# Kernel optimization log

Hardware: AMD Instinct MI355X
Metric: run time of the kernel (lower is better)

## Reference

```python
import jax, jax.numpy as jnp
import numpy as np

# dims
B, N = 8, 64            # graphs, nodes per graph (equal-size ragged batch)
IN_DIM, EDGE_DIM = 16, 8
D, H = 128, 4
DH = D // H             # 32
L = 3                   # num_layers
FF = 4 * D              # 512
OUT = 1
SCALE = float(np.sqrt(DH))


def setup_inputs() -> dict:
    key = jax.random.key(0)
    ks = jax.random.split(key, 24)
    w = lambda k, s: jax.random.normal(k, s, jnp.float32) * 0.02
    return {
        'x': jax.random.normal(ks[0], (B, N, IN_DIM), jnp.float32),
        'edge_attr': jax.random.normal(ks[1], (B, N, N, EDGE_DIM), jnp.float32),
        'edge_mask': jax.random.bernoulli(ks[2], 0.2, (B, N, N)),
        # feature encoder (linear node + linear edge encoders, learned no-edge token)
        'node_W': w(ks[3], (IN_DIM, D)), 'node_b': jnp.zeros((D,), jnp.float32),
        'edge_W': w(ks[4], (EDGE_DIM, D)), 'edge_b': jnp.zeros((D,), jnp.float32),
        'no_edge': w(ks[5], (D,)),
        # per-layer edge-transformer params (stacked over L for lax.scan)
        'Wq': w(ks[6], (L, D, D)), 'Wk': w(ks[7], (L, D, D)),
        'Wv1': w(ks[8], (L, D, D)), 'Wv2': w(ks[9], (L, D, D)),
        'Wo': w(ks[10], (L, D, D)), 'bo': jnp.zeros((L, D), jnp.float32),
        'ln1_g': jnp.ones((L, D), jnp.float32), 'ln1_b': jnp.zeros((L, D), jnp.float32),
        'W1': w(ks[11], (L, D, FF)), 'b1': jnp.zeros((L, FF), jnp.float32),
        'W2': w(ks[12], (L, FF, D)), 'b2': jnp.zeros((L, D), jnp.float32),
        'ln2_g': jnp.ones((L, D), jnp.float32), 'ln2_b': jnp.zeros((L, D), jnp.float32),
        'Wout': w(ks[13], (D, OUT)), 'bout': jnp.zeros((OUT,), jnp.float32),
    }


def _ln(t, g, b):
    m = t.mean(-1, keepdims=True)
    v = t.var(-1, keepdims=True)
    return (t - m) * jax.lax.rsqrt(v + 1e-5) * g + b


def _forward(x, edge_attr, edge_mask, node_W, node_b, edge_W, edge_b, no_edge,
             Wq, Wk, Wv1, Wv2, Wo, bo, ln1_g, ln1_b, W1, b1, W2, b2,
             ln2_g, ln2_b, Wout, bout):
    # feature encoding: pair-token grid [B,N,N,D]
    node_emb = x @ node_W + node_b                       # [B,N,D]
    edge_emb = edge_attr @ edge_W + edge_b               # [B,N,N,D]
    tok = jnp.where(edge_mask[..., None], edge_emb, no_edge)
    eye = jnp.eye(N, dtype=bool)
    tok = jnp.where(eye[None, :, :, None], node_emb[:, :, None, :], tok)

    def heads(t, W):
        return (t @ W).reshape(B, N, N, H, DH)

    def layer(tok, p):
        wq, wk, wv1, wv2, wo, bo_, g1, b1_, w1, bf1, w2, bf2, g2, b2_ = p
        q = heads(tok, wq); k = heads(tok, wk)
        v1 = heads(tok, wv1); v2 = heads(tok, wv2)
        # triangular attention: token (i,j) attends over intermediate l
        s = jnp.einsum('bilhd,bljhd->bhilj', q, k) / SCALE   # [B,H,N,N,N]
        a = jax.nn.softmax(s, axis=3)                        # softmax over l
        o = jnp.einsum('bhilj,bilhd,bljhd->bijhd', a, v1, v2).reshape(B, N, N, D)
        tok = _ln(tok + o @ wo + bo_, g1, b1_)
        f = jax.nn.relu(tok @ w1 + bf1) @ w2 + bf2
        tok = _ln(tok + f, g2, b2_)
        return tok, None

    tok, _ = jax.lax.scan(
        layer, tok,
        (Wq, Wk, Wv1, Wv2, Wo, bo, ln1_g, ln1_b, W1, b1, W2, b2, ln2_g, ln2_b))

    diag = tok[:, jnp.arange(N), jnp.arange(N), :]           # node tokens [B,N,D]
    return diag @ Wout + bout                                 # [B,N,OUT]


def reference(x, edge_attr, edge_mask, node_W, node_b, edge_W, edge_b, no_edge,
              Wq, Wk, Wv1, Wv2, Wo, bo, ln1_g, ln1_b, W1, b1, W2, b2,
              ln2_g, ln2_b, Wout, bout):
    return _forward(x, edge_attr, edge_mask, node_W, node_b, edge_W, edge_b,
                    no_edge, Wq, Wk, Wv1, Wv2, Wo, bo, ln1_g, ln1_b,
                    W1, b1, W2, b2, ln2_g, ln2_b, Wout, bout)
```

## Files before the change

kernel.cpp:

```cpp
#include <hip/hip_runtime.h>

typedef unsigned short u16;
typedef __attribute__((ext_vector_type(8))) short bf16x8;
typedef __attribute__((ext_vector_type(4))) float f32x4;

#define INV_SCALE 0.17677669529663687f

static __device__ __forceinline__ float b2f(u16 u) {
    union { unsigned int i; float f; } v; v.i = ((unsigned int)u) << 16; return v.f;
}
static __device__ __forceinline__ u16 f2b(float f) {
    union { float f; unsigned int i; } v; v.f = f;
    unsigned int r = (v.i + 0x7FFFu + ((v.i >> 16) & 1u)) >> 16;
    return (u16)r;
}

#define NSEG 23
__device__ __constant__ int d_seg_off[NSEG + 1] = {
    0, 8192, 270336, 272384, 272512, 273536, 273664, 273792, 322944, 372096,
    421248, 470400, 519552, 519936, 520320, 520704, 717312, 718848, 915456,
    915840, 916224, 916608, 916736, 916744};
static const int h_seg_off[NSEG + 1] = {
    0, 8192, 270336, 272384, 272512, 273536, 273664, 273792, 322944, 372096,
    421248, 470400, 519552, 519936, 520320, 520704, 717312, 718848, 915456,
    915840, 916224, 916608, 916736, 916744};
#define ARENA_TOTAL 916744

struct ParamPtrs { const void* p[NSEG]; };

__global__ __launch_bounds__(256) void convert_params(ParamPtrs pp, u16* __restrict__ arena,
                                                      const void* __restrict__ mask,
                                                      int* __restrict__ mode) {
    if (blockIdx.x == 0) {
        __shared__ int f16, f32s, u8s;
        int tid = threadIdx.x;
        if (tid == 0) { f16 = 0; f32s = 0; u8s = 0; }
        __syncthreads();
        const u16* mu = (const u16*)mask;
        const unsigned int* mw = (const unsigned int*)mask;
        if (mu[2 * tid] == 0x3F80u) atomicOr(&f16, 1);
        if (mw[tid] == 0x3F800000u) atomicOr(&f32s, 1);
        if (mw[tid] > 1u) atomicOr(&u8s, 1);
        __syncthreads();
        if (tid == 0) mode[0] = f16 ? 0 : (f32s ? 3 : (u8s ? 1 : 2));
    }
    const unsigned int probe = ((const unsigned int*)pp.p[13])[0];
    const bool f32 = (probe == 0x3F800000u);
    for (int e = blockIdx.x * 256 + threadIdx.x; e < ARENA_TOTAL; e += gridDim.x * 256) {
        int k = 0;
        #pragma unroll
        for (int s2 = 1; s2 < NSEG; ++s2) if (e >= d_seg_off[s2]) k = s2;
        int local = e - d_seg_off[k];
        u16 v;
        if (k == 22 && local >= 1) v = 0;
        else v = f32 ? f2b(((const float*)pp.p[k])[local]) : ((const u16*)pp.p[k])[local];
        arena[e] = v;
    }
}

__global__ __launch_bounds__(256) void assemble_kernel(
    const u16* __restrict__ x, const u16* __restrict__ ea,
    const void* __restrict__ mask, const int* __restrict__ modeptr,
    const u16* __restrict__ nodeW, const u16* __restrict__ nodeB,
    const u16* __restrict__ edgeW, const u16* __restrict__ edgeB, const u16* __restrict__ noedge,
    float* __restrict__ tokf, u16* __restrict__ tokb)
{
    const int md = modeptr[0];
    int g = blockIdx.x * 256 + threadIdx.x;
    int t = g >> 5, dq = g & 31, d0 = dq * 4;
    int b = t >> 12, i = (t >> 6) & 63, j = t & 63;
    float v[4];
    if (i == j) {
        #pragma unroll
        for (int c = 0; c < 4; c++) v[c] = b2f(nodeB[d0 + c]);
        #pragma unroll
        for (int e = 0; e < 16; e++) {
            float xe = b2f(x[(b * 64 + i) * 16 + e]);
            #pragma unroll
            for (int c = 0; c < 4; c++) v[c] += xe * b2f(nodeW[e * 128 + d0 + c]);
        }
    } else {
        bool edge;
        if (md == 0)      edge = ((const u16*)mask)[t] != 0;
        else if (md == 3) edge = ((const float*)mask)[t] != 0.0f;
        else if (md == 1) edge = ((const unsigned char*)mask)[t] != 0;
        else              edge = ((const unsigned int*)mask)[t] != 0;
        if (edge) {
            #pragma unroll
            for (int c = 0; c < 4; c++) v[c] = b2f(edgeB[d0 + c]);
            #pragma unroll
            for (int e = 0; e < 8; e++) {
                float ae = b2f(ea[t * 8 + e]);
                #pragma unroll
                for (int c = 0; c < 4; c++) v[c] += ae * b2f(edgeW[e * 128 + d0 + c]);
            }
        } else {
            #pragma unroll
            for (int c = 0; c < 4; c++) v[c] = b2f(noedge[d0 + c]);
        }
    }
    *(float4*)(tokf + (size_t)t * 128 + d0) = make_float4(v[0], v[1], v[2], v[3]);
    u16 pk[4];
    #pragma unroll
    for (int c = 0; c < 4; c++) pk[c] = f2b(v[c]);
    *(uint2*)(tokb + (size_t)t * 128 + d0) = *(uint2*)pk;
}

__global__ __launch_bounds__(512) void gemm_kernel(
    const u16* __restrict__ A, int lda,
    const u16* __restrict__ B0, const u16* __restrict__ B1,
    const u16* __restrict__ B2, const u16* __restrict__ B3,
    int ldb, const u16* __restrict__ bias,
    int K, int mode,
    u16* __restrict__ outb, int ldc,
    float* __restrict__ tokf,
    u16* __restrict__ qb, u16* __restrict__ kb, u16* __restrict__ v2b,
    const u16* __restrict__ lng, const u16* __restrict__ lnb, u16* __restrict__ tokbO)
{
    __shared__ __align__(16) u16 smem[2 * 128 * 72];
    u16* As = smem;
    u16* Bs = smem + 128 * 72;
    int tid = threadIdx.x;
    int m0 = blockIdx.x * 128;
    int by = blockIdx.y;
    const u16* Bp; int c0;
    if (mode == 3) { Bp = (by == 0) ? B0 : (by == 1) ? B1 : (by == 2) ? B2 : B3; c0 = 0; }
    else { Bp = B0; c0 = by * 128; }

    int w = tid >> 6, lane = tid & 63;
    int q = lane >> 4, r16 = lane & 15;
    int rw = (w >> 1) * 32, cw = (w & 1) * 64;

    f32x4 acc[2][4];
    #pragma unroll
    for (int mi = 0; mi < 2; mi++)
        #pragma unroll
        for (int ni = 0; ni < 4; ni++) acc[mi][ni] = (f32x4){0.f, 0.f, 0.f, 0.f};

    int nkt = K >> 6;
    for (int kt = 0; kt < nkt; ++kt) {
        int k0 = kt * 64;
        __syncthreads();
        #pragma unroll
        for (int it = 0; it < 2; ++it) {
            int idx = tid + it * 512;
            int row = idx >> 3, ch = idx & 7;
            uint4 d = *(const uint4*)(A + (size_t)(m0 + row) * lda + k0 + ch * 8);
            *(uint4*)&As[row * 72 + ch * 8] = d;
        }
        #pragma unroll
        for (int it = 0; it < 2; ++it) {
            int idx = tid + it * 512;
            int kk = idx >> 4, nc = idx & 15;
            uint4 d = *(const uint4*)(Bp + (size_t)(k0 + kk) * ldb + c0 + nc * 8);
            const u16* ds = (const u16*)&d;
            int chunk = kk >> 3, kin = kk & 7;
            #pragma unroll
            for (int e = 0; e < 8; ++e) {
                int n = nc * 8 + e;
                int ch2 = chunk ^ ((n >> 3) & 7);
                Bs[n * 72 + ch2 * 8 + kin] = ds[e];
            }
        }
        __syncthreads();
        #pragma unroll
        for (int ks = 0; ks < 2; ++ks) {
            bf16x8 fa[2], fb[4];
            #pragma unroll
            for (int mi = 0; mi < 2; mi++)
                fa[mi] = *(const bf16x8*)&As[(rw + mi * 16 + r16) * 72 + ks * 32 + q * 8];
            #pragma unroll
            for (int ni = 0; ni < 4; ni++) {
                int n = cw + ni * 16 + r16;
                int ch2 = (ks * 4 + q) ^ ((n >> 3) & 7);
                fb[ni] = *(const bf16x8*)&Bs[n * 72 + ch2 * 8];
            }
            #pragma unroll
            for (int mi = 0; mi < 2; mi++)
                #pragma unroll
                for (int ni = 0; ni < 4; ni++)
                    acc[mi][ni] = __builtin_amdgcn_mfma_f32_16x16x32_bf16(fa[mi], fb[ni], acc[mi][ni], 0, 0, 0);
        }
    }

    int bl = m0 >> 12, it0 = (m0 >> 6) & 63;
    __syncthreads();
    if (mode == 4) {
        float* cf  = (float*)smem;
        float* rsm = cf + 128 * 64;
        float* rqm = rsm + 256;
        int half = cw >> 6;
        #pragma unroll
        for (int ni = 0; ni < 4; ni++) {
            int col = cw + ni * 16 + r16;
            float bb = b2f(bias[col]);
            #pragma unroll
            for (int mi = 0; mi < 2; mi++)
                #pragma unroll
                for (int rr = 0; rr < 4; rr++) {
                    int r = rw + mi * 16 + q * 4 + rr;
                    acc[mi][ni][rr] += bb + tokf[(size_t)(m0 + r) * 128 + col];
                }
        }
        #pragma unroll
        for (int mi = 0; mi < 2; mi++)
            #pragma unroll
            for (int rr = 0; rr < 4; rr++) {
                float s = 0.f, sq = 0.f;
                #pragma unroll
                for (int ni = 0; ni < 4; ni++) { float t = acc[mi][ni][rr]; s += t; sq += t * t; }
                #pragma unroll
                for (int off = 1; off < 16; off <<= 1) {
                    s  += __shfl_xor(s,  off, 16);
                    sq += __shfl_xor(sq, off, 16);
                }
                if (r16 == 0) {
                    int r = rw + mi * 16 + q * 4 + rr;
                    rsm[half * 128 + r] = s;
                    rqm[half * 128 + r] = sq;
                }
            }
        __syncthreads();
        float gl[4], bv[4];
        #pragma unroll
        for (int ni = 0; ni < 4; ni++) {
            int col = cw + ni * 16 + r16;
            gl[ni] = b2f(lng[col]);
            bv[ni] = b2f(lnb[col]);
        }
        #pragma unroll
        for (int mi = 0; mi < 2; mi++)
            #pragma unroll
            for (int rr = 0; rr < 4; rr++) {
                int r = rw + mi * 16 + q * 4 + rr;
                float tot = rsm[r] + rsm[128 + r];
                float tq  = rqm[r] + rqm[128 + r];
                float mean = tot * 0.0078125f;
                float var  = tq * 0.0078125f - mean * mean;
                float rstd = rsqrtf(var + 1e-5f);
                #pragma unroll
                for (int ni = 0; ni < 4; ni++)
                    acc[mi][ni][rr] = (acc[mi][ni][rr] - mean) * rstd * gl[ni] + bv[ni];
            }
        #pragma unroll
        for (int hp = 0; hp < 2; ++hp) {
            __syncthreads();
            if (half == hp) {
                #pragma unroll
                for (int mi = 0; mi < 2; mi++)
                    #pragma unroll
                    for (int ni = 0; ni < 4; ni++) {
                        int colh = (cw & 63) + ni * 16 + r16;
                        int ch4 = colh >> 2, cl = colh & 3;
                        #pragma unroll
                        for (int rr = 0; rr < 4; rr++) {
                            int r = rw + mi * 16 + q * 4 + rr;
                            cf[r * 64 + (((ch4 ^ (r & 15)) << 2) | cl)] = acc[mi][ni][rr];
                        }
                    }
            }
            __syncthreads();
            #pragma unroll
            for (int it = 0; it < 4; ++it) {
                int idx = tid + it * 512;
                int r = idx >> 4, c4 = idx & 15;
                f32x4 v = *(const f32x4*)&cf[r * 64 + ((c4 ^ (r & 15)) << 2)];
                int col = hp * 64 + c4 * 4;
                *(f32x4*)(tokf + (size_t)(m0 + r) * 128 + col) = v;
                u16 pk[4];
                #pragma unroll
                for (int e = 0; e < 4; e++) pk[e] = f2b(v[e]);
                *(uint2*)(tokbO + (size_t)(m0 + r) * 128 + col) = *(uint2*)pk;
            }
        }
    } else if (mode == 3 && by == 2) {
        float* cf = (float*)smem;
        #pragma unroll
        for (int hp = 0; hp < 2; ++hp) {
            if (hp) __syncthreads();
            if ((cw >> 6) == hp) {
                #pragma unroll
                for (int mi = 0; mi < 2; mi++) {
                    #pragma unroll
                    for (int ni = 0; ni < 4; ni++) {
                        int colh = (cw & 63) + ni * 16 + r16;
                        int ch4 = colh >> 2, cl = colh & 3;
                        #pragma unroll
                        for (int rr = 0; rr < 4; rr++) {
                            int r = rw + mi * 16 + q * 4 + rr;
                            cf[r * 64 + (((ch4 ^ (r & 15)) << 2) | cl)] = acc[mi][ni][rr];
                        }
                    }
                }
            }
            __syncthreads();
            #pragma unroll
            for (int it = 0; it < 4; ++it) {
                int idx = tid + it * 512;
                int hh = idx >> 10, itl = (idx >> 9) & 1, jt = (idx >> 3) & 63, d4 = idx & 7;
                int r = itl * 64 + jt;
                int colh = hh * 32 + d4 * 4;
                f32x4 v = *(const f32x4*)&cf[r * 64 + (((colh >> 2) ^ (r & 15)) << 2)];
                int h = hp * 2 + hh;
                *(f32x4*)&tokf[((((size_t)(bl * 4 + h)) * 64 + it0 + itl) * 64 + jt) * 32 + d4 * 4] = v;
            }
        }
    } else {
        u16* cs = smem;
        #pragma unroll
        for (int mi = 0; mi < 2; mi++) {
            #pragma unroll
            for (int ni = 0; ni < 4; ni++) {
                int col = cw + ni * 16 + r16;
                int ch = col >> 3, cl = col & 7;
                #pragma unroll
                for (int rr = 0; rr < 4; rr++) {
                    int r = rw + mi * 16 + q * 4 + rr;
                    cs[r * 128 + (((ch ^ (r & 15)) << 3) | cl)] = f2b(acc[mi][ni][rr]);
                }
            }
        }
        __syncthreads();
        if (by == 0) {
            #pragma unroll
            for (int it = 0; it < 4; ++it) {
                int idx = tid + it * 512;
                int h = idx >> 9, jt = (idx >> 3) & 63, itl = (idx >> 2) & 1, d8 = idx & 3;
                int r = itl * 64 + jt, c8 = h * 4 + d8;
                uint4 d = *(const uint4*)&cs[r * 128 + ((c8 ^ (r & 15)) << 3)];
                *(uint4*)&qb[((((size_t)(bl * 4 + h)) * 64 + jt) * 64 + it0 + itl) * 32 + d8 * 8] = d;
            }
        } else {
            u16* dp = (by == 1) ? kb : v2b;
            #pragma unroll
            for (int it = 0; it < 4; ++it) {
                int idx = tid + it * 512;
                int h = idx >> 9, itl = (idx >> 8) & 1, jt = (idx >> 2) & 63, d8 = idx & 3;
                int r = itl * 64 + jt, c8 = h * 4 + d8;
                uint4 d = *(const uint4*)&cs[r * 128 + ((c8 ^ (r & 15)) << 3)];
                *(uint4*)&dp[((((size_t)(bl * 4 + h)) * 64 + it0 + itl) * 64 + jt) * 32 + d8 * 8] = d;
            }
        }
    }
}

__global__ __launch_bounds__(512) void ff_kernel(
    const u16* __restrict__ A,
    const u16* __restrict__ W1, const u16* __restrict__ b1,
    const u16* __restrict__ W2, const u16* __restrict__ b2,
    const u16* __restrict__ lng, const u16* __restrict__ lnb,
    float* __restrict__ tokf, u16* __restrict__ tokbO)
{
    __shared__ __align__(16) u16 smem[2 * 128 * 72];
    u16* As = smem;
    u16* Bs = smem + 128 * 72;
    int tid = threadIdx.x;
    int m0 = blockIdx.x * 128;
    int w = tid >> 6, lane = tid & 63;
    int q = lane >> 4, r16 = lane & 15;
    int rw = (w >> 1) * 32, cw = (w & 1) * 64;

    f32x4 acc2[2][4];
    #pragma unroll
    for (int mi = 0; mi < 2; mi++)
        #pragma unroll
        for (int ni = 0; ni < 4; ni++) acc2[mi][ni] = (f32x4){0.f, 0.f, 0.f, 0.f};

    for (int hs = 0; hs < 4; ++hs) {
        f32x4 acc1[2][4];
        #pragma unroll
        for (int mi = 0; mi < 2; mi++)
            #pragma unroll
            for (int ni = 0; ni < 4; ni++) acc1[mi][ni] = (f32x4){0.f, 0.f, 0.f, 0.f};
        #pragma unroll
        for (int kt = 0; kt < 2; ++kt) {
            int k0 = kt * 64;
            __syncthreads();
            #pragma unroll
            for (int it = 0; it < 2; ++it) {
                int idx = tid + it * 512;
                int row = idx >> 3, ch = idx & 7;
                uint4 d = *(const uint4*)(A + (size_t)(m0 + row) * 128 + k0 + ch * 8);
                *(uint4*)&As[row * 72 + ch * 8] = d;
            }
            #pragma unroll
            for (int it = 0; it < 2; ++it) {
                int idx = tid + it * 512;
                int kk = idx >> 4, nc = idx & 15;
                uint4 d = *(const uint4*)(W1 + (size_t)(k0 + kk) * 512 + hs * 128 + nc * 8);
                const u16* ds = (const u16*)&d;
                int chunk = kk >> 3, kin = kk & 7;
                #pragma unroll
                for (int e = 0; e < 8; ++e) {
                    int n = nc * 8 + e;
                    int ch2 = chunk ^ ((n >> 3) & 7);
                    Bs[n * 72 + ch2 * 8 + kin] = ds[e];
                }
            }
            __syncthreads();
            #pragma unroll
            for (int ks = 0; ks < 2; ++ks) {
                bf16x8 fa[2], fb[4];
                #pragma unroll
                for (int mi = 0; mi < 2; mi++)
                    fa[mi] = *(const bf16x8*)&As[(rw + mi * 16 + r16) * 72 + ks * 32 + q * 8];
                #pragma unroll
                for (int ni = 0; ni < 4; ni++) {
                    int n = cw + ni * 16 + r16;
                    int ch2 = (ks * 4 + q) ^ ((n >> 3) & 7);
                    fb[ni] = *(const bf16x8*)&Bs[n * 72 + ch2 * 8];
                }
                #pragma unroll
                for (int mi = 0; mi < 2; mi++)
                    #pragma unroll
                    for (int ni = 0; ni < 4; ni++)
                        acc1[mi][ni] = __builtin_amdgcn_mfma_f32_16x16x32_bf16(fa[mi], fb[ni], acc1[mi][ni], 0, 0, 0);
            }
        }
        #pragma unroll
        for (int half = 0; half < 2; ++half) {
            __syncthreads();
            if ((w & 1) == half) {
                #pragma unroll
                for (int mi = 0; mi < 2; mi++)
                    #pragma unroll
                    for (int ni = 0; ni < 4; ni++) {
                        int kl = ni * 16 + r16;
                        float bb = b2f(b1[hs * 128 + half * 64 + kl]);
                        #pragma unroll
                        for (int rr = 0; rr < 4; rr++) {
                            int row = rw + mi * 16 + q * 4 + rr;
                            As[row * 72 + kl] = f2b(fmaxf(acc1[mi][ni][rr] + bb, 0.f));
                        }
                    }
            }
            #pragma unroll
            for (int it = 0; it < 2; ++it) {
                int idx = tid + it * 512;
                int kk = idx >> 4, nc = idx & 15;
                uint4 d = *(const uint4*)(W2 + (size_t)(hs * 128 + half * 64 + kk) * 128 + nc * 8);
                const u16* ds = (const u16*)&d;
                int chunk = kk >> 3, kin = kk & 7;
                #pragma unroll
                for (int e = 0; e < 8; ++e) {
                    int n = nc * 8 + e;
                    int ch2 = chunk ^ ((n >> 3) & 7);
                    Bs[n * 72 + ch2 * 8 + kin] = ds[e];
                }
            }
            __syncthreads();
            #pragma unroll
            for (int ks = 0; ks < 2; ++ks) {
                bf16x8 fa[2], fb[4];
                #pragma unroll
                for (int mi = 0; mi < 2; mi++)
                    fa[mi] = *(const bf16x8*)&As[(rw + mi * 16 + r16) * 72 + ks * 32 + q * 8];
                #pragma unroll
                for (int ni = 0; ni < 4; ni++) {
                    int n = cw + ni * 16 + r16;
                    int ch2 = (ks * 4 + q) ^ ((n >> 3) & 7);
                    fb[ni] = *(const bf16x8*)&Bs[n * 72 + ch2 * 8];
                }
                #pragma unroll
                for (int mi = 0; mi < 2; mi++)
                    #pragma unroll
                    for (int ni = 0; ni < 4; ni++)
                        acc2[mi][ni] = __builtin_amdgcn_mfma_f32_16x16x32_bf16(fa[mi], fb[ni], acc2[mi][ni], 0, 0, 0);
            }
        }
    }

    __syncthreads();
    float* cf  = (float*)smem;
    float* rsm = cf + 128 * 64;
    float* rqm = rsm + 256;
    int half = cw >> 6;
    #pragma unroll
    for (int ni = 0; ni < 4; ni++) {
        int col = cw + ni * 16 + r16;
        float bb = b2f(b2[col]);
        #pragma unroll
        for (int mi = 0; mi < 2; mi++)
            #pragma unroll
            for (int rr = 0; rr < 4; rr++) {
                int r = rw + mi * 16 + q * 4 + rr;
                acc2[mi][ni][rr] += bb + tokf[(size_t)(m0 + r) * 128 + col];
            }
    }
    #pragma unroll
    for (int mi = 0; mi < 2; mi++)
        #pragma unroll
        for (int rr = 0; rr < 4; rr++) {
            float s = 0.f, sq = 0.f;
            #pragma unroll
            for (int ni = 0; ni < 4; ni++) { float t = acc2[mi][ni][rr]; s += t; sq += t * t; }
            #pragma unroll
            for (int off = 1; off < 16; off <<= 1) {
                s  += __shfl_xor(s,  off, 16);
                sq += __shfl_xor(sq, off, 16);
            }
            if (r16 == 0) {
                int r = rw + mi * 16 + q * 4 + rr;
                rsm[half * 128 + r] = s;
                rqm[half * 128 + r] = sq;
            }
        }
    __syncthreads();
    float gl[4], bv[4];
    #pragma unroll
    for (int ni = 0; ni < 4; ni++) {
        int col = cw + ni * 16 + r16;
        gl[ni] = b2f(lng[col]);
        bv[ni] = b2f(lnb[col]);
    }
    #pragma unroll
    for (int mi = 0; mi < 2; mi++)
        #pragma unroll
        for (int rr = 0; rr < 4; rr++) {
            int r = rw + mi * 16 + q * 4 + rr;
            float tot = rsm[r] + rsm[128 + r];
            float tq  = rqm[r] + rqm[128 + r];
            float mean = tot * 0.0078125f;
            float var  = tq * 0.0078125f - mean * mean;
            float rstd = rsqrtf(var + 1e-5f);
            #pragma unroll
            for (int ni = 0; ni < 4; ni++)
                acc2[mi][ni][rr] = (acc2[mi][ni][rr] - mean) * rstd * gl[ni] + bv[ni];
        }
    #pragma unroll
    for (int hp = 0; hp < 2; ++hp) {
        __syncthreads();
        if (half == hp) {
            #pragma unroll
            for (int mi = 0; mi < 2; mi++)
                #pragma unroll
                for (int ni = 0; ni < 4; ni++) {
                    int colh = (cw & 63) + ni * 16 + r16;
                    int ch4 = colh >> 2, cl = colh & 3;
                    #pragma unroll
                    for (int rr = 0; rr < 4; rr++) {
                        int r = rw + mi * 16 + q * 4 + rr;
                        cf[r * 64 + (((ch4 ^ (r & 15)) << 2) | cl)] = acc2[mi][ni][rr];
                    }
                }
        }
        __syncthreads();
        #pragma unroll
        for (int it = 0; it < 4; ++it) {
            int idx = tid + it * 512;
            int r = idx >> 4, c4 = idx & 15;
            f32x4 v = *(const f32x4*)&cf[r * 64 + ((c4 ^ (r & 15)) << 2)];
            int col = hp * 64 + c4 * 4;
            *(f32x4*)(tokf + (size_t)(m0 + r) * 128 + col) = v;
            u16 pk[4];
            #pragma unroll
            for (int e = 0; e < 4; e++) pk[e] = f2b(v[e]);
            *(uint2*)(tokbO + (size_t)(m0 + r) * 128 + col) = *(uint2*)pk;
        }
    }
}

__global__ __launch_bounds__(64) void attn_s_kernel(
    const u16* __restrict__ qb, const u16* __restrict__ kb, u16* __restrict__ s)
{
    __shared__ __align__(16) u16 sm[64 * 80];
    u16* qs  = sm;
    u16* ks_ = sm + 64 * 40;
    int g = blockIdx.x;
    int l = g & 63, bh = g >> 6;
    const u16* Q = qb + ((size_t)bh * 64 + l) * 2048;
    const u16* Kp = kb + ((size_t)bh * 64 + l) * 2048;
    int lane = threadIdx.x;
    #pragma unroll
    for (int it = 0; it < 4; ++it) {
        int idx = lane + it * 64;
        int row = idx >> 2, c4 = idx & 3;
        *(uint4*)&qs[row * 40 + c4 * 8] = *(const uint4*)(Q + row * 32 + c4 * 8);
        *(uint4*)&ks_[row * 40 + c4 * 8] = *(const uint4*)(Kp + row * 32 + c4 * 8);
    }
    __syncthreads();
    int q = lane >> 4, r16 = lane & 15;
    f32x4 acc[4][4];
    #pragma unroll
    for (int mi = 0; mi < 4; mi++)
        #pragma unroll
        for (int ni = 0; ni < 4; ni++) acc[mi][ni] = (f32x4){0.f, 0.f, 0.f, 0.f};
    bf16x8 fa[4], fb[4];
    #pragma unroll
    for (int mi = 0; mi < 4; mi++) fa[mi] = *(const bf16x8*)&qs[(mi * 16 + r16) * 40 + q * 8];
    #pragma unroll
    for (int ni = 0; ni < 4; ni++) fb[ni] = *(const bf16x8*)&ks_[(ni * 16 + r16) * 40 + q * 8];
    #pragma unroll
    for (int mi = 0; mi < 4; mi++)
        #pragma unroll
        for (int ni = 0; ni < 4; ni++)
            acc[mi][ni] = __builtin_amdgcn_mfma_f32_16x16x32_bf16(fa[mi], fb[ni], acc[mi][ni], 0, 0, 0);
    __syncthreads();
    u16* cs = sm;
    #pragma unroll
    for (int mi = 0; mi < 4; mi++)
        #pragma unroll
        for (int ni = 0; ni < 4; ni++)
            #pragma unroll
            for (int rr = 0; rr < 4; rr++)
                cs[(mi * 16 + q * 4 + rr) * 72 + ni * 16 + r16] = f2b(acc[mi][ni][rr] * INV_SCALE);
    __syncthreads();
    u16* sb = s + (size_t)bh * 262144 + l * 64;
    #pragma unroll
    for (int it = 0; it < 8; ++it) {
        int row = it * 8 + (lane >> 3);
        uint4 d = *(const uint4*)&cs[row * 72 + (lane & 7) * 8];
        *(uint4*)&sb[(size_t)row * 4096 + (lane & 7) * 8] = d;
    }
}

__global__ __launch_bounds__(256) void attn_o_kernel(
    const u16* __restrict__ a, const float* __restrict__ v1f, const u16* __restrict__ v2b,
    u16* __restrict__ ob)
{
    __shared__ __align__(16) float v2s[4 * 1152];
    __shared__ __align__(16) u16   as_[8 * 4 * 32];
    __shared__ __align__(16) float v1s[8 * 4 * 32];
    int bh = blockIdx.x;
    int i0 = blockIdx.y * 8;
    int jh = blockIdx.z;
    int bl = bh >> 2, h = bh & 3;
    int tid = threadIdx.x;
    int j32 = tid & 31;
    int ih = (tid >> 5) & 1;
    int dh = (tid >> 6) * 8;
    int jg = jh * 32 + j32;
    const u16*   v2base = v2b + (size_t)bh * 131072;
    const float* v1base = v1f + (size_t)bh * 131072 + (size_t)i0 * 2048;
    const u16*   abase  = a + (size_t)bh * 262144 + (size_t)i0 * 4096;

    int lz[2], jz[2], cz[2];
    #pragma unroll
    for (int it = 0; it < 2; ++it) {
        int idx = tid + it * 256;
        lz[it] = idx >> 7; jz[it] = (idx >> 2) & 31; cz[it] = idx & 3;
    }
    int ia = tid >> 5, la = (tid >> 3) & 3, jaq = tid & 7;
    int iv = tid >> 5, lv = (tid >> 3) & 3, dvq = (tid & 7) * 4;

    uint4 pv2[2]; uint2 pa; f32x4 pv1;

#define LOAD_CHUNK(l0_)                                                             \
    _Pragma("unroll")                                                               \
    for (int it = 0; it < 2; ++it)                                                  \
        pv2[it] = *(const uint4*)(v2base + ((size_t)((l0_) + lz[it]) * 64 + jh * 32 + jz[it]) * 32 + cz[it] * 8); \
    pa  = *(const uint2*)(abase + (size_t)ia * 4096 + ((l0_) + la) * 64 + jh * 32 + jaq * 4); \
    pv1 = *(const f32x4*)(v1base + (size_t)iv * 2048 + ((l0_) + lv) * 32 + dvq);

#define STORE_CHUNK()                                                               \
    _Pragma("unroll")                                                               \
    for (int it = 0; it < 2; ++it) {                                                \
        const u16* ds = (const u16*)&pv2[it];                                       \
        float* dst = &v2s[lz[it] * 1152 + jz[it] * 36 + cz[it] * 8];                \
        _Pragma("unroll")                                                           \
        for (int e = 0; e < 8; e++) dst[e] = b2f(ds[e]);                            \
    }                                                                               \
    *(uint2*)&as_[ia * 128 + la * 32 + jaq * 4] = pa;                               \
    *(f32x4*)&v1s[iv * 128 + lv * 32 + dvq] = pv1;

    float acc[4][8];
    float Z[4];
    #pragma unroll
    for (int i = 0; i < 4; i++) {
        Z[i] = 0.f;
        #pragma unroll
        for (int e = 0; e < 8; e++) acc[i][e] = 0.f;
    }

    LOAD_CHUNK(0);
    for (int ch = 0; ch < 16; ++ch) {
        if (ch) __syncthreads();
        STORE_CHUNK();
        if (ch + 1 < 16) LOAD_CHUNK((ch + 1) * 4);
        __syncthreads();
        #pragma unroll
        for (int lc = 0; lc < 4; ++lc) {
            const float* vp = &v2s[lc * 1152 + j32 * 36 + dh];
            float v2r[8];
            *(f32x4*)&v2r[0] = *(const f32x4*)vp;
            *(f32x4*)&v2r[4] = *(const f32x4*)(vp + 4);
            #pragma unroll
            for (int ii = 0; ii < 4; ++ii) {
                int iL = ih * 4 + ii;
                float sv = b2f(as_[iL * 128 + lc * 32 + j32]);
                float av = __expf(sv);
                Z[ii] += av;
                const float* v1p = &v1s[iL * 128 + lc * 32 + dh];
                #pragma unroll
                for (int e = 0; e < 8; e++)
                    acc[ii][e] += (av * v1p[e]) * v2r[e];
            }
        }
    }
#undef LOAD_CHUNK
#undef STORE_CHUNK

    #pragma unroll
    for (int ii = 0; ii < 4; ++ii) {
        int iL = ih * 4 + ii;
        float sc = 1.0f / Z[ii];
        u16 tmp[8];
        #pragma unroll
        for (int e = 0; e < 8; e++) tmp[e] = f2b(acc[ii][e] * sc);
        *(uint4*)(ob + ((size_t)(bl * 64 + i0 + iL) * 64 + jg) * 128 + h * 32 + dh) = *(uint4*)tmp;
    }
}

__global__ __launch_bounds__(256) void out_kernel(
    const float* __restrict__ tokf, const u16* __restrict__ Wout, const u16* __restrict__ bout,
    float* __restrict__ out)
{
    int g = blockIdx.x * 256 + threadIdx.x;
    int b = g >> 6, i = g & 63;
    const float* p = tokf + ((size_t)(b * 64 + i) * 64 + i) * 128;
    float s = b2f(bout[0]);
    #pragma unroll
    for (int d = 0; d < 128; d++) s += p[d] * b2f(Wout[d]);
    out[g] = s;
}

extern "C" void kernel_launch(void* const* d_in, const int* in_sizes, int n_in,
                              void* d_out, int out_size, void* d_ws, size_t ws_size,
                              hipStream_t stream) {
    const void* mask = d_in[2];
    ParamPtrs pp;
    for (int k = 0; k < NSEG; ++k) pp.p[k] = d_in[k < 2 ? k : k + 1];

    char* ws = (char*)d_ws;
    u16* arena = (u16*)ws;
    #define AP(k) ((const u16*)ws + h_seg_off[k])
    int*   mmode = (int*)(ws + 1835008);
    float* tokf  = (float*)(ws + 2097152);
    u16*   tokb  = (u16*)(ws + 18874368);
    const size_t base = 27262976;
    const size_t MB = 1048576ULL;

    int NB = 8;
    while (NB > 1 && base + (size_t)NB * 7 * MB > ws_size) NB >>= 1;

    u16*   qb  = (u16*)(ws + base);
    u16*   kb  = (u16*)(ws + base + (size_t)NB * MB);
    u16*   v2b = (u16*)(ws + base + (size_t)NB * 2 * MB);
    float* v1f = (float*)(ws + base + (size_t)NB * 3 * MB);
    u16*   sb  = (u16*)(ws + base + (size_t)NB * 5 * MB);
    u16*   ob  = qb;

    convert_params<<<1024, 256, 0, stream>>>(pp, arena, mask, mmode);
    assemble_kernel<<<4096, 256, 0, stream>>>(AP(0), AP(1), mask, mmode,
                                              AP(2), AP(3), AP(4), AP(5), AP(6), tokf, tokb);

    for (int l = 0; l < 3; ++l) {
        const u16* Wq_l  = AP(7)  + l * 16384;
        const u16* Wk_l  = AP(8)  + l * 16384;
        const u16* Wv1_l = AP(9)  + l * 16384;
        const u16* Wv2_l = AP(10) + l * 16384;
        const u16* Wo_l  = AP(11) + l * 16384;
        const u16* bo_l  = AP(12) + l * 128;
        const u16* g1_l  = AP(13) + l * 128;
        const u16* be1_l = AP(14) + l * 128;
        const u16* W1_l  = AP(15) + l * 65536;
        const u16* b1_l  = AP(16) + l * 512;
        const u16* W2_l  = AP(17) + l * 65536;
        const u16* b2_l  = AP(18) + l * 128;
        const u16* g2_l  = AP(19) + l * 128;
        const u16* be2_l = AP(20) + l * 128;

        for (int r = 0; r < 8 / NB; ++r) {
            size_t rowOff = (size_t)r * NB * 4096;
            gemm_kernel<<<dim3(NB * 32, 4), 512, 0, stream>>>(
                tokb + rowOff * 128, 128, Wq_l, Wk_l, Wv1_l, Wv2_l,
                128, (const u16*)0, 128, 3, (u16*)0, 0, v1f, qb, kb, v2b,
                (const u16*)0, (const u16*)0, (u16*)0);
            attn_s_kernel<<<NB * 256, 64, 0, stream>>>(qb, kb, sb);
            attn_o_kernel<<<dim3(NB * 4, 8, 2), 256, 0, stream>>>(sb, v1f, v2b, ob);
            gemm_kernel<<<dim3(NB * 32, 1), 512, 0, stream>>>(
                ob, 128, Wo_l, (const u16*)0, (const u16*)0, (const u16*)0,
                128, bo_l, 128, 4, (u16*)0, 0, tokf + rowOff * 128,
                (u16*)0, (u16*)0, (u16*)0,
                g1_l, be1_l, tokb + rowOff * 128);
        }
        ff_kernel<<<256, 512, 0, stream>>>(tokb, W1_l, b1_l, W2_l, b2_l,
                                           g2_l, be2_l, tokf, tokb);
    }
    out_kernel<<<2, 256, 0, stream>>>(tokf, AP(21), AP(22), (float*)d_out);
}
```

Measured before the change: 408.3 us.

## Pre-transpose weights in arena and halve GEMM row tiles to 64

The arena packing kernel now stores the Wq/Wk/Wv1/Wv2/Wo, W1 and W2 weights transposed (N-major, K contiguous). The GEMM and FF kernels can then load B tiles with vectorized 16-byte stores into swizzled shared memory instead of scattering eight scalar writes per load. Separately, the row tile shrinks from 128 to 64 with 256-thread blocks and twice as many blocks, which cuts shared memory per block and raises block count. Epilogue indexing for the q/k/v scatter and LayerNorm reductions is adjusted to match, at the cost of re-reading B weights twice as often across blocks.

```diff
diff --git a/kernel.cpp b/kernel.cpp
--- a/kernel.cpp
+++ b/kernel.cpp
@@ -51,9 +51,23 @@
         #pragma unroll
         for (int s2 = 1; s2 < NSEG; ++s2) if (e >= d_seg_off[s2]) k = s2;
         int local = e - d_seg_off[k];
+        int src = local;
+        if (k >= 7 && k <= 11) {
+            int l = local >> 14, rem = local & 16383;
+            int n = rem >> 7, kk = rem & 127;
+            src = (l << 14) + kk * 128 + n;
+        } else if (k == 15) {
+            int l = local >> 16, rem = local & 65535;
+            int n = rem >> 7, kk = rem & 127;
+            src = (l << 16) + kk * 512 + n;
+        } else if (k == 17) {
+            int l = local >> 16, rem = local & 65535;
+            int n = rem >> 9, kk = rem & 511;
+            src = (l << 16) + kk * 128 + n;
+        }
         u16 v;
         if (k == 22 && local >= 1) v = 0;
-        else v = f32 ? f2b(((const float*)pp.p[k])[local]) : ((const u16*)pp.p[k])[local];
+        else v = f32 ? f2b(((const float*)pp.p[k])[src]) : ((const u16*)pp.p[k])[src];
         arena[e] = v;
     }
 }
@@ -106,26 +120,25 @@
     *(uint2*)(tokb + (size_t)t * 128 + d0) = *(uint2*)pk;
 }
 
-__global__ __launch_bounds__(512) void gemm_kernel(
+__global__ __launch_bounds__(256) void gemm_kernel(
     const u16* __restrict__ A, int lda,
     const u16* __restrict__ B0, const u16* __restrict__ B1,
     const u16* __restrict__ B2, const u16* __restrict__ B3,
-    int ldb, const u16* __restrict__ bias,
+    int ldbt, const u16* __restrict__ bias,
     int K, int mode,
-    u16* __restrict__ outb, int ldc,
     float* __restrict__ tokf,
     u16* __restrict__ qb, u16* __restrict__ kb, u16* __restrict__ v2b,
     const u16* __restrict__ lng, const u16* __restrict__ lnb, u16* __restrict__ tokbO)
 {
-    __shared__ __align__(16) u16 smem[2 * 128 * 72];
+    __shared__ __align__(16) u16 smem[64 * 72 + 128 * 72];
     u16* As = smem;
-    u16* Bs = smem + 128 * 72;
+    u16* Bs = smem + 64 * 72;
     int tid = threadIdx.x;
-    int m0 = blockIdx.x * 128;
+    int m0 = blockIdx.x * 64;
     int by = blockIdx.y;
-    const u16* Bp; int c0;
-    if (mode == 3) { Bp = (by == 0) ? B0 : (by == 1) ? B1 : (by == 2) ? B2 : B3; c0 = 0; }
-    else { Bp = B0; c0 = by * 128; }
+    const u16* Bp;
+    if (mode == 3) { Bp = (by == 0) ? B0 : (by == 1) ? B1 : (by == 2) ? B2 : B3; }
+    else { Bp = B0; }
 
     int w = tid >> 6, lane = tid & 63;
     int q = lane >> 4, r16 = lane & 15;
@@ -143,24 +156,18 @@
         __syncthreads();
         #pragma unroll
         for (int it = 0; it < 2; ++it) {
-            int idx = tid + it * 512;
+            int idx = tid + it * 256;
             int row = idx >> 3, ch = idx & 7;
             uint4 d = *(const uint4*)(A + (size_t)(m0 + row) * lda + k0 + ch * 8);
             *(uint4*)&As[row * 72 + ch * 8] = d;
         }
         #pragma unroll
-        for (int it = 0; it < 2; ++it) {
-            int idx = tid + it * 512;
-            int kk = idx >> 4, nc = idx & 15;
-            uint4 d = *(const uint4*)(Bp + (size_t)(k0 + kk) * ldb + c0 + nc * 8);
-            const u16* ds = (const u16*)&d;
-            int chunk = kk >> 3, kin = kk & 7;
-            #pragma unroll
-            for (int e = 0; e < 8; ++e) {
-                int n = nc * 8 + e;
-                int ch2 = chunk ^ ((n >> 3) & 7);
-                Bs[n * 72 + ch2 * 8 + kin] = ds[e];
-            }
+        for (int it = 0; it < 4; ++it) {
+            int idx = tid + it * 256;
+            int n = idx >> 3, ch = idx & 7;
+            uint4 d = *(const uint4*)(Bp + (size_t)n * ldbt + k0 + ch * 8);
+            int ch2 = ch ^ ((n >> 3) & 7);
+            *(uint4*)&Bs[n * 72 + ch2 * 8] = d;
         }
         __syncthreads();
         #pragma unroll
@@ -187,8 +194,8 @@
     __syncthreads();
     if (mode == 4) {
         float* cf  = (float*)smem;
-        float* rsm = cf + 128 * 64;
-        float* rqm = rsm + 256;
+        float* rsm = cf + 64 * 64;
+        float* rqm = rsm + 128;
         int half = cw >> 6;
         #pragma unroll
         for (int ni = 0; ni < 4; ni++) {
@@ -216,8 +223,8 @@
                 }
                 if (r16 == 0) {
                     int r = rw + mi * 16 + q * 4 + rr;
-                    rsm[half * 128 + r] = s;
-                    rqm[half * 128 + r] = sq;
+                    rsm[half * 64 + r] = s;
+                    rqm[half * 64 + r] = sq;
                 }
             }
         __syncthreads();
@@ -233,8 +240,8 @@
             #pragma unroll
             for (int rr = 0; rr < 4; rr++) {
                 int r = rw + mi * 16 + q * 4 + rr;
-                float tot = rsm[r] + rsm[128 + r];
-                float tq  = rqm[r] + rqm[128 + r];
+                float tot = rsm[r] + rsm[64 + r];
+                float tq  = rqm[r] + rqm[64 + r];
                 float mean = tot * 0.0078125f;
                 float var  = tq * 0.0078125f - mean * mean;
                 float rstd = rsqrtf(var + 1e-5f);
@@ -262,7 +269,7 @@
             __syncthreads();
             #pragma unroll
             for (int it = 0; it < 4; ++it) {
-                int idx = tid + it * 512;
+                int idx = tid + it * 256;
                 int r = idx >> 4, c4 = idx & 15;
                 f32x4 v = *(const f32x4*)&cf[r * 64 + ((c4 ^ (r & 15)) << 2)];
                 int col = hp * 64 + c4 * 4;
@@ -296,13 +303,12 @@
             __syncthreads();
             #pragma unroll
             for (int it = 0; it < 4; ++it) {
-                int idx = tid + it * 512;
-                int hh = idx >> 10, itl = (idx >> 9) & 1, jt = (idx >> 3) & 63, d4 = idx & 7;
-                int r = itl * 64 + jt;
+                int idx = tid + it * 256;
+                int hh = idx >> 9, r = (idx >> 3) & 63, d4 = idx & 7;
                 int colh = hh * 32 + d4 * 4;
                 f32x4 v = *(const f32x4*)&cf[r * 64 + (((colh >> 2) ^ (r & 15)) << 2)];
                 int h = hp * 2 + hh;
-                *(f32x4*)&tokf[((((size_t)(bl * 4 + h)) * 64 + it0 + itl) * 64 + jt) * 32 + d4 * 4] = v;
+                *(f32x4*)&tokf[((((size_t)(bl * 4 + h)) * 64 + it0) * 64 + r) * 32 + d4 * 4] = v;
             }
         }
     } else {
@@ -324,38 +330,38 @@
         if (by == 0) {
             #pragma unroll
             for (int it = 0; it < 4; ++it) {
-                int idx = tid + it * 512;
-                int h = idx >> 9, jt = (idx >> 3) & 63, itl = (idx >> 2) & 1, d8 = idx & 3;
-                int r = itl * 64 + jt, c8 = h * 4 + d8;
+                int idx = tid + it * 256;
+                int h = idx >> 8, r = (idx >> 2) & 63, d8 = idx & 3;
+                int c8 = h * 4 + d8;
                 uint4 d = *(const uint4*)&cs[r * 128 + ((c8 ^ (r & 15)) << 3)];
-                *(uint4*)&qb[((((size_t)(bl * 4 + h)) * 64 + jt) * 64 + it0 + itl) * 32 + d8 * 8] = d;
+                *(uint4*)&qb[((((size_t)(bl * 4 + h)) * 64 + r) * 64 + it0) * 32 + d8 * 8] = d;
             }
         } else {
             u16* dp = (by == 1) ? kb : v2b;
             #pragma unroll
             for (int it = 0; it < 4; ++it) {
-                int idx = tid + it * 512;
-                int h = idx >> 9, itl = (idx >> 8) & 1, jt = (idx >> 2) & 63, d8 = idx & 3;
-                int r = itl * 64 + jt, c8 = h * 4 + d8;
+                int idx = tid + it * 256;
+                int h = idx >> 8, r = (idx >> 2) & 63, d8 = idx & 3;
+                int c8 = h * 4 + d8;
                 uint4 d = *(const uint4*)&cs[r * 128 + ((c8 ^ (r & 15)) << 3)];
-                *(uint4*)&dp[((((size_t)(bl * 4 + h)) * 64 + it0 + itl) * 64 + jt) * 32 + d8 * 8] = d;
-            }
-        }
-    }
-}
-
-__global__ __launch_bounds__(512) void ff_kernel(
+                *(uint4*)&dp[((((size_t)(bl * 4 + h)) * 64 + it0) * 64 + r) * 32 + d8 * 8] = d;
+            }
+        }
+    }
+}
+
+__global__ __launch_bounds__(256) void ff_kernel(
     const u16* __restrict__ A,
-    const u16* __restrict__ W1, const u16* __restrict__ b1,
-    const u16* __restrict__ W2, const u16* __restrict__ b2,
+    const u16* __restrict__ W1T, const u16* __restrict__ b1,
+    const u16* __restrict__ W2T, const u16* __restrict__ b2,
     const u16* __restrict__ lng, const u16* __restrict__ lnb,
     float* __restrict__ tokf, u16* __restrict__ tokbO)
 {
-    __shared__ __align__(16) u16 smem[2 * 128 * 72];
+    __shared__ __align__(16) u16 smem[64 * 72 + 128 * 72];
     u16* As = smem;
-    u16* Bs = smem + 128 * 72;
+    u16* Bs = smem + 64 * 72;
     int tid = threadIdx.x;
-    int m0 = blockIdx.x * 128;
+    int m0 = blockIdx.x * 64;
     int w = tid >> 6, lane = tid & 63;
     int q = lane >> 4, r16 = lane & 15;
     int rw = (w >> 1) * 32, cw = (w & 1) * 64;
@@ -378,24 +384,18 @@
             __syncthreads();
             #pragma unroll
             for (int it = 0; it < 2; ++it) {
-                int idx = tid + it * 512;
+                int idx = tid + it * 256;
                 int row = idx >> 3, ch = idx & 7;
                 uint4 d = *(const uint4*)(A + (size_t)(m0 + row) * 128 + k0 + ch * 8);
                 *(uint4*)&As[row * 72 + ch * 8] = d;
             }
             #pragma unroll
-            for (int it = 0; it < 2; ++it) {
-                int idx = tid + it * 512;
-                int kk = idx >> 4, nc = idx & 15;
-                uint4 d = *(const uint4*)(W1 + (size_t)(k0 + kk) * 512 + hs * 128 + nc * 8);
-                const u16* ds = (const u16*)&d;
-                int chunk = kk >> 3, kin = kk & 7;
-                #pragma unroll
-                for (int e = 0; e < 8; ++e) {
-                    int n = nc * 8 + e;
-                    int ch2 = chunk ^ ((n >> 3) & 7);
-                    Bs[n * 72 + ch2 * 8 + kin] = ds[e];
-                }
+            for (int it = 0; it < 4; ++it) {
+                int idx = tid + it * 256;
+                int n = idx >> 3, ch = idx & 7;
+                uint4 d = *(const uint4*)(W1T + (size_t)(hs * 128 + n) * 128 + k0 + ch * 8);
+                int ch2 = ch ^ ((n >> 3) & 7);
+                *(uint4*)&Bs[n * 72 + ch2 * 8] = d;
             }
             __syncthreads();
             #pragma unroll
@@ -435,18 +435,12 @@
                     }
             }
             #pragma unroll
-            for (int it = 0; it < 2; ++it) {
-                int idx = tid + it * 512;
-                int kk = idx >> 4, nc = idx & 15;
-                uint4 d = *(const uint4*)(W2 + (size_t)(hs * 128 + half * 64 + kk) * 128 + nc * 8);
-                const u16* ds = (const u16*)&d;
-                int chunk = kk >> 3, kin = kk & 7;
-                #pragma unroll
-                for (int e = 0; e < 8; ++e) {
-                    int n = nc * 8 + e;
-                    int ch2 = chunk ^ ((n >> 3) & 7);
-                    Bs[n * 72 + ch2 * 8 + kin] = ds[e];
-                }
+            for (int it = 0; it < 4; ++it) {
+                int idx = tid + it * 256;
+                int n = idx >> 3, ch = idx & 7;
+                uint4 d = *(const uint4*)(W2T + (size_t)n * 512 + hs * 128 + half * 64 + ch * 8);
+                int ch2 = ch ^ ((n >> 3) & 7);
+                *(uint4*)&Bs[n * 72 + ch2 * 8] = d;
             }
             __syncthreads();
             #pragma unroll
@@ -472,8 +466,8 @@
 
     __syncthreads();
     float* cf  = (float*)smem;
-    float* rsm = cf + 128 * 64;
-    float* rqm = rsm + 256;
+    float* rsm = cf + 64 * 64;
+    float* rqm = rsm + 128;
     int half = cw >> 6;
     #pragma unroll
     for (int ni = 0; ni < 4; ni++) {
@@ -501,8 +495,8 @@
             }
             if (r16 == 0) {
                 int r = rw + mi * 16 + q * 4 + rr;
-                rsm[half * 128 + r] = s;
-                rqm[half * 128 + r] = sq;
+                rsm[half * 64 + r] = s;
+                rqm[half * 64 + r] = sq;
             }
         }
     __syncthreads();
@@ -518,8 +512,8 @@
         #pragma unroll
         for (int rr = 0; rr < 4; rr++) {
             int r = rw + mi * 16 + q * 4 + rr;
-            float tot = rsm[r] + rsm[128 + r];
-            float tq  = rqm[r] + rqm[128 + r];
+            float tot = rsm[r] + rsm[64 + r];
+            float tq  = rqm[r] + rqm[64 + r];
             float mean = tot * 0.0078125f;
             float var  = tq * 0.0078125f - mean * mean;
             float rstd = rsqrtf(var + 1e-5f);
@@ -547,7 +541,7 @@
         __syncthreads();
         #pragma unroll
         for (int it = 0; it < 4; ++it) {
-            int idx = tid + it * 512;
+            int idx = tid + it * 256;
             int r = idx >> 4, c4 = idx & 15;
             f32x4 v = *(const f32x4*)&cf[r * 64 + ((c4 ^ (r & 15)) << 2)];
             int col = hp * 64 + c4 * 4;
@@ -772,19 +766,19 @@
 
         for (int r = 0; r < 8 / NB; ++r) {
             size_t rowOff = (size_t)r * NB * 4096;
-            gemm_kernel<<<dim3(NB * 32, 4), 512, 0, stream>>>(
+            gemm_kernel<<<dim3(NB * 64, 4), 256, 0, stream>>>(
                 tokb + rowOff * 128, 128, Wq_l, Wk_l, Wv1_l, Wv2_l,
-                128, (const u16*)0, 128, 3, (u16*)0, 0, v1f, qb, kb, v2b,
+                128, (const u16*)0, 128, 3, v1f, qb, kb, v2b,
                 (const u16*)0, (const u16*)0, (u16*)0);
             attn_s_kernel<<<NB * 256, 64, 0, stream>>>(qb, kb, sb);
             attn_o_kernel<<<dim3(NB * 4, 8, 2), 256, 0, stream>>>(sb, v1f, v2b, ob);
-            gemm_kernel<<<dim3(NB * 32, 1), 512, 0, stream>>>(
+            gemm_kernel<<<dim3(NB * 64, 1), 256, 0, stream>>>(
                 ob, 128, Wo_l, (const u16*)0, (const u16*)0, (const u16*)0,
-                128, bo_l, 128, 4, (u16*)0, 0, tokf + rowOff * 128,
+                128, bo_l, 128, 4, tokf + rowOff * 128,
                 (u16*)0, (u16*)0, (u16*)0,
                 g1_l, be1_l, tokb + rowOff * 128);
         }
-        ff_kernel<<<256, 512, 0, stream>>>(tokb, W1_l, b1_l, W2_l, b2_l,
+        ff_kernel<<<512, 256, 0, stream>>>(tokb, W1_l, b1_l, W2_l, b2_l,
                                            g2_l, be2_l, tokf, tokb);
     }
     out_kernel<<<2, 256, 0, stream>>>(tokf, AP(21), AP(22), (float*)d_out);
```

Result: no change. 413.0 us (+1.1%).
